# Kernel optimization log

Hardware: AMD Instinct MI355X
Metric: run time of the kernel (lower is better)

The kernel has to match this reference:

```python
import jax, jax.numpy as jnp
import numpy as np

B, N, E = 16, 512, 131072
FEAT, EMB, H = 3, 512, 3
K1, K2 = 410, 205  # ceil(0.8*512), ceil(0.5*410) per PyG TopKPooling
NEG_SLOPE, EPS = 0.2, 1e-5


def _gat_conv(x, W, att_s, att_d, bias, src, tgt, valid, num_nodes):
    # PyG GATConv (concat=True): per-edge attention with segment softmax over targets.
    Hh, C = att_s.shape
    xp = (x @ W).reshape(-1, Hh, C)                      # [Nn,H,C]
    a_s = jnp.einsum('nhc,hc->nh', xp, att_s)
    a_d = jnp.einsum('nhc,hc->nh', xp, att_d)
    srcc = jnp.where(valid, src, 0)
    tgtc = jnp.where(valid, tgt, 0)
    e = jax.nn.leaky_relu(a_s[srcc] + a_d[tgtc], NEG_SLOPE)  # [Ee,H]
    seg = jnp.where(valid, tgt, num_nodes)               # invalid edges -> dummy segment
    emax = jax.ops.segment_max(e, seg, num_segments=num_nodes + 1)
    emax = jnp.where(jnp.isfinite(emax), emax, 0.0)
    ex = jnp.exp(e - emax[seg]) * valid[:, None].astype(e.dtype)
    den = jax.ops.segment_sum(ex, seg, num_segments=num_nodes + 1)
    alpha = ex / jnp.maximum(den[seg], 1e-16)            # [Ee,H]
    out = jax.ops.segment_sum(alpha[:, :, None] * xp[srcc], seg,
                              num_segments=num_nodes + 1)[:num_nodes]
    return out.reshape(num_nodes, Hh * C) + bias


def _bn(x, g, b):
    # BatchNorm1d, training-mode batch statistics (biased var), eps=1e-5
    m = x.mean(0)
    v = x.var(0)
    return (x - m) * jax.lax.rsqrt(v + EPS) * g + b


def _topk_pool(x, p, nb, n_per, k):
    # PyG TopKPooling: score = tanh(x.w/||w||), keep top-k per graph, scale by score
    score = jnp.tanh((x @ p) / jnp.linalg.norm(p))       # [nb*n_per]
    top_s, top_i = jax.lax.top_k(score.reshape(nb, n_per), k)
    perm = (top_i + jnp.arange(nb)[:, None] * n_per).reshape(-1)
    x_new = x[perm] * top_s.reshape(-1, 1)
    mapping = jnp.full((nb * n_per,), -1, jnp.int32).at[perm].set(
        jnp.arange(nb * k, dtype=jnp.int32))
    return x_new, mapping


def _pool_cat(x, nb, k):
    # [global_max_pool, global_mean_pool] over equal-size graphs
    xr = x.reshape(nb, k, -1)
    return jnp.concatenate([xr.max(1), xr.mean(1)], axis=1)


def _forward(x, W1, as1, ad1, bc1, Wh1, bh1, g1, be1, p1,
             W2, as2, ad2, bc2, Wh2, bh2, g2, be2, p2,
             Wl1, bl1, Wl2, bl2, edge_index):
    Nn = B * N
    src0, tgt0 = edge_index[0], edge_index[1]
    sl = jnp.arange(Nn, dtype=jnp.int32)                 # GATConv add_self_loops=True
    src1 = jnp.concatenate([src0, sl]); tgt1 = jnp.concatenate([tgt0, sl])
    valid1 = jnp.ones(src1.shape, bool)
    h = _gat_conv(x, W1, as1, ad1, bc1, src1, tgt1, valid1, Nn)
    h = jax.nn.relu(h @ Wh1 + bh1)
    h = _bn(h, g1, be1)
    h, mapping = _topk_pool(h, p1, B, N, K1)
    x1 = _pool_cat(h, B, K1)                             # [B, 2*EMB]
    # relabel edges to pooled node ids; drop edges with removed endpoints via mask
    s2 = mapping[src0]; t2 = mapping[tgt0]
    v2 = (s2 >= 0) & (t2 >= 0)
    sl2 = jnp.arange(B * K1, dtype=jnp.int32)
    src2 = jnp.concatenate([s2, sl2]); tgt2 = jnp.concatenate([t2, sl2])
    valid2 = jnp.concatenate([v2, jnp.ones(sl2.shape, bool)])
    h = _gat_conv(h, W2, as2, ad2, bc2, src2, tgt2, valid2, B * K1)
    h = jax.nn.relu(h @ Wh2 + bh2)
    h = _bn(h, g2, be2)
    h, _ = _topk_pool(h, p2, B, K1, K2)
    x2 = _pool_cat(h, B, K2)
    xg = x1 + x2
    xg = jax.nn.relu(xg @ Wl1 + bl1)                     # dropout p=0.5 disabled (eval)
    return xg @ Wl2 + bl2                                # [B, 256]


def setup_inputs() -> dict:
    key = jax.random.key(0)
    ks = jax.random.split(key, 16)
    x = jax.random.normal(ks[0], (B * N, FEAT), jnp.float32)
    goff = jnp.repeat(jnp.arange(B, dtype=jnp.int32), E // B) * N
    src = jax.random.randint(ks[1], (E,), 0, N, jnp.int32) + goff
    tgt = jax.random.randint(ks[2], (E,), 0, N, jnp.int32) + goff
    edge_index = jnp.stack([src, tgt])
    s = 0.05
    p = {
        'W1': jax.random.normal(ks[3], (FEAT, H * EMB)) * s,
        'as1': jax.random.normal(ks[4], (H, EMB)) * s,
        'ad1': jax.random.normal(ks[5], (H, EMB)) * s,
        'bc1': jnp.zeros((H * EMB,)),
        'Wh1': jax.random.normal(ks[6], (H * EMB, EMB)) * s,
        'bh1': jnp.zeros((EMB,)),
        'g1': jnp.ones((EMB,)), 'be1': jnp.zeros((EMB,)),
        'p1': jax.random.normal(ks[7], (EMB,)) * s,
        'W2': jax.random.normal(ks[8], (EMB, H * EMB)) * s,
        'as2': jax.random.normal(ks[9], (H, EMB)) * s,
        'ad2': jax.random.normal(ks[10], (H, EMB)) * s,
        'bc2': jnp.zeros((H * EMB,)),
        'Wh2': jax.random.normal(ks[11], (H * EMB, EMB)) * s,
        'bh2': jnp.zeros((EMB,)),
        'g2': jnp.ones((EMB,)), 'be2': jnp.zeros((EMB,)),
        'p2': jax.random.normal(ks[12], (EMB,)) * s,
        'Wl1': jax.random.normal(ks[13], (2 * EMB, 512)) * s,
        'bl1': jnp.zeros((512,)),
        'Wl2': jax.random.normal(ks[14], (512, 256)) * s,
        'bl2': jnp.zeros((256,)),
    }
    return {'x': x, 'edge_index': edge_index, **p}


def reference(x, edge_index, W1, as1, ad1, bc1, Wh1, bh1, g1, be1, p1,
              W2, as2, ad2, bc2, Wh2, bh2, g2, be2, p2, Wl1, bl1, Wl2, bl2):
    return _forward(x, W1, as1, ad1, bc1, Wh1, bh1, g1, be1, p1,
                    W2, as2, ad2, bc2, Wh2, bh2, g2, be2, p2,
                    Wl1, bl1, Wl2, bl2, edge_index)
```

## Files before the change

### kernel.cpp

```cpp
#include <hip/hip_runtime.h>
#include <hip/hip_bf16.h>
#include <math.h>

#define E_EDGES 131072
#define NN1 8192
#define NN2 6560
#define NG 16
#define NP1 512
#define KP1 410
#define KP2 205
#define F1 1536
#define EMB 512
#define MAXDEG 256
#define BNCH 256

typedef __hip_bfloat16 bf16;
typedef __attribute__((ext_vector_type(8))) short short8;
typedef __attribute__((ext_vector_type(4))) float f32x4;
typedef __attribute__((ext_vector_type(4))) unsigned short us4;

__device__ inline float wred64(float v){
  #pragma unroll
  for (int o = 32; o; o >>= 1) v += __shfl_down(v, o);
  return v;
}
__device__ inline float b2f_raw(unsigned short u){
  return __uint_as_float((unsigned)u << 16);
}
union BFU { bf16 b; unsigned short u; };
__device__ inline unsigned short f2u(float v){ BFU x; x.b = __float2bfloat16(v); return x.u; }

__device__ __forceinline__ void gld16(const void* g, void* l){
  __builtin_amdgcn_global_load_lds(
      (const __attribute__((address_space(1))) void*)g,
      (__attribute__((address_space(3))) void*)l, 16, 0, 0);
}

__device__ inline void split_store(float v, bf16* __restrict__ ph, bf16* __restrict__ pl){
  bf16 hi = __float2bfloat16(v);
  *ph = hi;
  *pl = __float2bfloat16(v - __bfloat162float(hi));
}

__device__ inline void bn_tail(float s, float q, int c, float* __restrict__ stats,
    int M, const float* __restrict__ p, float* __restrict__ pnout){
  float mean = s / (float)M;
  float var = fmaxf(q / (float)M - mean*mean, 0.f);
  stats[c] = mean;
  stats[512+c] = 1.f / sqrtf(var + 1e-5f);
  float v = p[c]; v = v*v;
  v = wred64(v);
  __shared__ float red[8];
  int lane = c & 63, wv = c >> 6;
  if (lane == 0) red[wv] = v;
  __syncthreads();
  if (c == 0){ float sm = 0.f; for (int i = 0; i < 8; i++) sm += red[i]; pnout[0] = sqrtf(sm); }
}

__global__ __launch_bounds__(256) void k_pre(
    const float* __restrict__ W1, const float* __restrict__ as1, const float* __restrict__ ad1,
    const float* __restrict__ Wh1, const float* __restrict__ bc1, const float* __restrict__ bh1,
    const float* __restrict__ W2, const float* __restrict__ as2, const float* __restrict__ ad2,
    const float* __restrict__ Wh2, const float* __restrict__ bc2, const float* __restrict__ bh2,
    float* __restrict__ was1, float* __restrict__ wad1, float* __restrict__ M1p,
    float* __restrict__ cvp,
    float* __restrict__ was2, float* __restrict__ wad2,
    int* __restrict__ cnt1, int* __restrict__ cnt2, int* __restrict__ map,
    float* __restrict__ bnacc, float* __restrict__ bnacc1){
  int b = blockIdx.x, t = threadIdx.x;
  if (b < 24){
    int h = b / 8, rem = b % 8, jh = rem >> 2, kc = rem & 3;
    int j = jh*256 + t, c0 = kc*128;
    __shared__ float w1s[3][128];
    for (int i = t; i < 384; i += 256)
      w1s[i>>7][i&127] = W1[(i>>7)*1536 + h*512 + c0 + (i&127)];
    __syncthreads();
    const float* whc = Wh1 + (size_t)(h*512 + c0)*512 + j;
    float a0=0.f, a1=0.f, a2=0.f;
    #pragma unroll 8
    for (int c = 0; c < 128; c++){
      float v = whc[(size_t)c*512];
      a0 += w1s[0][c]*v; a1 += w1s[1][c]*v; a2 += w1s[2][c]*v;
    }
    float* dst = M1p + (size_t)kc*4608;
    dst[(h*3+0)*512 + j] = a0;
    dst[(h*3+1)*512 + j] = a1;
    dst[(h*3+2)*512 + j] = a2;
  } else if (b < 56){
    int b2 = b - 24;
    int which = b2 >> 4, rem = b2 & 15, jh = rem >> 3, kc = rem & 7;
    const float* bc = which ? bc2 : bc1;
    const float* Wh = which ? Wh2 : Wh1;
    const float* bh = which ? bh2 : bh1;
    int j = jh*256 + t, i0 = kc*192;
    float acc = (kc == 0) ? bh[j] : 0.f;
    #pragma unroll 8
    for (int i = 0; i < 192; i++)
      acc += bc[i0+i] * Wh[(size_t)(i0+i)*512 + j];
    cvp[(size_t)(which*8 + kc)*512 + j] = acc;
  } else if (b < 152){
    int b3 = b - 56;
    int y = b3 >> 4, et = b3 & 15;
    int kind = y / 3, h = y % 3;
    int w = t >> 6, lane = t & 63;
    const float* att = kind ? ad2 : as2;
    float a[8];
    #pragma unroll
    for (int u = 0; u < 8; u++) a[u] = att[h*512 + lane*8 + u];
    for (int r = w; r < 32; r += 4){
      int e = et*32 + r;
      const float4* row = (const float4*)(W2 + (size_t)e*1536 + h*512) + lane*2;
      float4 v0 = row[0], v1 = row[1];
      float d = v0.x*a[0]+v0.y*a[1]+v0.z*a[2]+v0.w*a[3]
              + v1.x*a[4]+v1.y*a[5]+v1.z*a[6]+v1.w*a[7];
      d = wred64(d);
      if (lane == 0) (kind ? wad2 : was2)[h*512 + e] = d;
    }
  } else if (b < 170){
    if (t < 64){
      int bb = b - 152;
      int kind = bb / 9, r = bb % 9, h = r / 3, f = r % 3;
      const float* att = kind ? ad1 : as1;
      float s = 0.f;
      for (int c = t; c < 512; c += 64) s += W1[f*1536 + h*512 + c] * att[h*512 + c];
      s = wred64(s);
      if (t == 0) (kind ? wad1 : was1)[h*3 + f] = s;
    }
  } else {
    int i = (b - 170)*256 + t;
    if (i < NN1){ cnt1[i] = 1; map[i] = -1; }
    if (i < NN2){ cnt2[i] = 1; }
    if (i < 1024){ bnacc[i] = 0.f; bnacc1[i] = 0.f; }
  }
}

__global__ __launch_bounds__(256) void k_gemm_s_mfma(const float* __restrict__ A0,
    const float* __restrict__ B0, bf16* __restrict__ Th, bf16* __restrict__ Tl){
  int z = blockIdx.z;
  const float* A = A0 + (size_t)z*512;
  const float* B = B0 + (size_t)z*512*512;
  __shared__ __align__(16) short sAh[4096], sAl[4096], sBh[4096], sBl[4096];
  int t = threadIdx.x, w = t >> 6, lane = t & 63;
  int l16 = lane & 15, q = lane >> 4;
  int bm = blockIdx.y*64, bn = blockIdx.x*64;

  int am  = t >> 2, akw = (t & 3)*16;
  int bnl = t & 63, bkq = (t >> 6)*16;

  f32x4 acc[4];
  #pragma unroll
  for (int nf = 0; nf < 4; nf++) acc[nf] = (f32x4){0.f,0.f,0.f,0.f};

  float va[16], vb[16];
  #define GS_LOAD(K0) do { \
    _Pragma("unroll") for (int u = 0; u < 4; u++){ \
      float4 v4 = *(const float4*)(A + (size_t)(bm+am)*1536 + (K0) + akw + u*4); \
      va[u*4]=v4.x; va[u*4+1]=v4.y; va[u*4+2]=v4.z; va[u*4+3]=v4.w; } \
    _Pragma("unroll") for (int u = 0; u < 16; u++) \
      vb[u] = B[(size_t)((K0) + bkq + u)*512 + bn + bnl]; \
  } while(0)

  GS_LOAD(0);
  for (int it = 0; it < 8; it++){
    #pragma unroll
    for (int hh = 0; hh < 2; hh++){
      short8 ah_, al_, bh_, bl_;
      #pragma unroll
      for (int jj = 0; jj < 8; jj++){
        float v = va[hh*8+jj];
        unsigned short hu = f2u(v);
        ah_[jj] = (short)hu; al_[jj] = (short)f2u(v - b2f_raw(hu));
        v = vb[hh*8+jj];
        hu = f2u(v);
        bh_[jj] = (short)hu; bl_[jj] = (short)f2u(v - b2f_raw(hu));
      }
      int aoff = am*64  + ((((akw>>3) + hh) ^ (am  & 7)) << 3);
      *(short8*)(sAh + aoff) = ah_;
      *(short8*)(sAl + aoff) = al_;
      int boff = bnl*64 + ((((bkq>>3) + hh) ^ (bnl & 7)) << 3);
      *(short8*)(sBh + boff) = bh_;
      *(short8*)(sBl + boff) = bl_;
    }
    __syncthreads();
    if (it < 7) GS_LOAD((it+1)*64);
    #pragma unroll
    for (int ks = 0; ks < 2; ks++){
      int gc = ks*4 + q;
      int ar = w*16 + l16;
      int ao = ar*64 + ((gc ^ (ar & 7)) << 3);
      short8 afh = *(const short8*)(sAh + ao);
      short8 afl = *(const short8*)(sAl + ao);
      #pragma unroll
      for (int nf = 0; nf < 4; nf++){
        int br = nf*16 + l16;
        int bo = br*64 + ((gc ^ (br & 7)) << 3);
        short8 bfh = *(const short8*)(sBh + bo);
        short8 bfl = *(const short8*)(sBl + bo);
        acc[nf] = __builtin_amdgcn_mfma_f32_16x16x32_bf16(afh, bfh, acc[nf], 0, 0, 0);
        acc[nf] = __builtin_amdgcn_mfma_f32_16x16x32_bf16(afh, bfl, acc[nf], 0, 0, 0);
        acc[nf] = __builtin_amdgcn_mfma_f32_16x16x32_bf16(afl, bfh, acc[nf], 0, 0, 0);
      }
    }
    __syncthreads();
  }
  #undef GS_LOAD

  int m0 = bm + w*16 + q*4;
  #pragma unroll
  for (int nf = 0; nf < 4; nf++){
    int n = bn + nf*16 + l16;
    size_t base = (size_t)n*1536 + (size_t)z*512 + m0;
    #pragma unroll
    for (int e = 0; e < 4; e++)
      split_store(acc[nf][e], &Th[base+e], &Tl[base+e]);
  }
}

__global__ void k_count1(const int* __restrict__ tgt0, int* __restrict__ cnt, int E){
  int i = blockIdx.x*blockDim.x + threadIdx.x;
  if (i < E) atomicAdd(&cnt[tgt0[i]], 1);
}
__global__ void k_count2(const int* __restrict__ src0, const int* __restrict__ tgt0,
                         const int* __restrict__ map, int* __restrict__ cnt, int E){
  int i = blockIdx.x*blockDim.x + threadIdx.x;
  if (i >= E) return;
  int s = map[src0[i]], tg = map[tgt0[i]];
  if (s >= 0 && tg >= 0) atomicAdd(&cnt[tg], 1);
}
__global__ __launch_bounds__(1024) void k_scan(const int* __restrict__ counts,
    int* __restrict__ off, int* __restrict__ cur, int n){
  __shared__ int sh[1024];
  int t = threadIdx.x;
  int chunk = (n + 1023) >> 10;
  int b = t * chunk; int e = b + chunk; if (e > n) e = n;
  int s = 0;
  for (int i = b; i < e && i < n; i++) s += counts[i];
  sh[t] = s; __syncthreads();
  for (int o = 1; o < 1024; o <<= 1){
    int v = (t >= o) ? sh[t-o] : 0;
    __syncthreads();
    sh[t] += v;
    __syncthreads();
  }
  int run = (t > 0) ? sh[t-1] : 0;
  for (int i = b; i < e && i < n; i++){ int c = counts[i]; off[i] = run; cur[i] = run; run += c; }
  if (t == 1023) off[n] = sh[1023];
}
__global__ void k_fill1(const int* __restrict__ src0, const int* __restrict__ tgt0,
                        int* __restrict__ cur, int* __restrict__ esrc, int E, int nn){
  int i = blockIdx.x*blockDim.x + threadIdx.x;
  if (i >= E + nn) return;
  int s, tg;
  if (i < E){ s = src0[i]; tg = tgt0[i]; } else { s = i - E; tg = s; }
  int pos = atomicAdd(&cur[tg], 1);
  esrc[pos] = s;
}
__global__ void k_fill2(const int* __restrict__ src0, const int* __restrict__ tgt0,
                        const int* __restrict__ map, int* __restrict__ cur,
                        int* __restrict__ esrc, int E, int nn){
  int i = blockIdx.x*blockDim.x + threadIdx.x;
  if (i >= E + nn) return;
  int s, tg;
  if (i < E){
    s = map[src0[i]]; tg = map[tgt0[i]];
    if (s < 0 || tg < 0) return;
  } else { s = i - E; tg = s; }
  int pos = atomicAdd(&cur[tg], 1);
  esrc[pos] = s;
}

__global__ __launch_bounds__(64) void k_agg1(
    const float* __restrict__ x, const int* __restrict__ off, const int* __restrict__ esrc,
    const float* __restrict__ was, const float* __restrict__ wad,
    float* __restrict__ aggx){
  int n = blockIdx.x, t = threadIdx.x;
  __shared__ float xs[MAXDEG][3];
  __shared__ float al[MAXDEG*3];
  __shared__ float mh[3], dh[3];
  int s0 = off[n]; int deg = off[n+1] - s0; if (deg > MAXDEG) deg = MAXDEG;
  float ad0, ad1, ad2;
  {
    float x0 = x[n*3], x1 = x[n*3+1], x2 = x[n*3+2];
    ad0 = x0*wad[0] + x1*wad[1] + x2*wad[2];
    ad1 = x0*wad[3] + x1*wad[4] + x2*wad[5];
    ad2 = x0*wad[6] + x1*wad[7] + x2*wad[8];
  }
  for (int e = t; e < deg; e += 64){
    int s = esrc[s0 + e];
    float x0 = x[s*3], x1 = x[s*3+1], x2 = x[s*3+2];
    xs[e][0] = x0; xs[e][1] = x1; xs[e][2] = x2;
    float v0 = x0*was[0] + x1*was[1] + x2*was[2] + ad0;
    float v1 = x0*was[3] + x1*was[4] + x2*was[5] + ad1;
    float v2 = x0*was[6] + x1*was[7] + x2*was[8] + ad2;
    al[e*3+0] = v0 > 0.f ? v0 : 0.2f*v0;
    al[e*3+1] = v1 > 0.f ? v1 : 0.2f*v1;
    al[e*3+2] = v2 > 0.f ? v2 : 0.2f*v2;
  }
  __syncthreads();
  if (t < 3){
    float m = -INFINITY;
    for (int e = 0; e < deg; e++) m = fmaxf(m, al[e*3+t]);
    float d = 0.f;
    for (int e = 0; e < deg; e++) d += expf(al[e*3+t] - m);
    mh[t] = m; dh[t] = 1.f / fmaxf(d, 1e-16f);
  }
  __syncthreads();
  float acc[9] = {0,0,0,0,0,0,0,0,0};
  for (int e = t; e < deg; e += 64){
    #pragma unroll
    for (int h = 0; h < 3; h++){
      float a = expf(al[e*3+h] - mh[h]) * dh[h];
      acc[h*3+0] += a * xs[e][0];
      acc[h*3+1] += a * xs[e][1];
      acc[h*3+2] += a * xs[e][2];
    }
  }
  #pragma unroll
  for (int q = 0; q < 9; q++){
    float v = wred64(acc[q]);
    if (t == 0) aggx[(size_t)n*9 + q] = v;
  }
}

__global__ __launch_bounds__(256) void k_h1(const float* __restrict__ aggx,
    const float* __restrict__ M1p, const float* __restrict__ cvp1, bf16* __restrict__ hout,
    float* __restrict__ bnacc1){
  __shared__ float sM[9*512];
  __shared__ float sC[512];
  __shared__ float sA[32*9];
  int t = threadIdx.x; int n0 = blockIdx.x*32;
  for (int i = t; i < 9*512; i += 256)
    sM[i] = M1p[i] + M1p[4608 + i] + M1p[2*4608 + i] + M1p[3*4608 + i];
  for (int i = t; i < 512; i += 256){
    float s = 0.f;
    #pragma unroll
    for (int kc = 0; kc < 8; kc++) s += cvp1[kc*512 + i];
    sC[i] = s;
  }
  for (int i = t; i < 288; i += 256) sA[i] = aggx[(size_t)n0*9 + i];
  __syncthreads();
  float c0v = sC[t], c1v = sC[t+256];
  float ls0=0.f, lq0=0.f, ls1=0.f, lq1=0.f;
  #pragma unroll 4
  for (int i = 0; i < 32; i++){
    float a0 = c0v, a1 = c1v;
    #pragma unroll
    for (int q = 0; q < 9; q++){
      float av = sA[i*9+q];
      a0 += av * sM[q*512 + t];
      a1 += av * sM[q*512 + t + 256];
    }
    a0 = fmaxf(a0, 0.f); a1 = fmaxf(a1, 0.f);
    hout[(size_t)(n0+i)*512 + t]       = __float2bfloat16(a0);
    hout[(size_t)(n0+i)*512 + t + 256] = __float2bfloat16(a1);
    ls0 += a0; lq0 += a0*a0; ls1 += a1; lq1 += a1*a1;
  }
  atomicAdd(&bnacc1[t],           ls0);
  atomicAdd(&bnacc1[t+256],       ls1);
  atomicAdd(&bnacc1[512 + t],     lq0);
  atomicAdd(&bnacc1[512 + t+256], lq1);
}

__global__ void k_bn_final_1(const float* __restrict__ bnacc,
    float* __restrict__ stats, int M, const float* __restrict__ p, float* __restrict__ pnout){
  int c = threadIdx.x;
  bn_tail(bnacc[c], bnacc[512 + c], c, stats, M, p, pnout);
}
__global__ __launch_bounds__(256) void k_score(
    const bf16* __restrict__ h, const float* __restrict__ stats,
    const float* __restrict__ g_, const float* __restrict__ be,
    const float* __restrict__ p, const float* __restrict__ pn,
    float* __restrict__ score){
  int r = blockIdx.x, t = threadIdx.x;
  float dot = 0.f;
  #pragma unroll
  for (int k = 0; k < 2; k++){
    int c = t + k*256;
    float v = (__bfloat162float(h[(size_t)r*EMB + c]) - stats[c]) * stats[512+c] * g_[c] + be[c];
    dot += v * p[c];
  }
  dot = wred64(dot);
  __shared__ float red[4];
  int lane = t & 63, wv = t >> 6;
  if (lane == 0) red[wv] = dot;
  __syncthreads();
  if (t == 0) score[r] = tanhf((red[0]+red[1]+red[2]+red[3]) / pn[0]);
}

__global__ __launch_bounds__(512) void k_topk_sort(
    const float* __restrict__ score, int* __restrict__ map,
    int* __restrict__ topi, float* __restrict__ tops, int n_per, int K){
  int g = blockIdx.x, t = threadIdx.x;
  __shared__ float sk[512];
  __shared__ int si[512];
  if (t < n_per){ sk[t] = score[g*n_per + t]; si[t] = t; }
  else { sk[t] = -INFINITY; si[t] = 0x7fffffff; }
  __syncthreads();
  for (int k = 2; k <= 512; k <<= 1){
    for (int j = k >> 1; j > 0; j >>= 1){
      int l = t ^ j;
      if (l > t){
        float ki = sk[t], kl = sk[l]; int ii = si[t], il = si[l];
        bool before_l = (kl > ki) || (kl == ki && il < ii);
        bool up = ((t & k) == 0);
        if (up == before_l){ sk[t]=kl; sk[l]=ki; si[t]=il; si[l]=ii; }
      }
      __syncthreads();
    }
  }
  if (t < K){
    if (map) map[g*n_per + si[t]] = g*K + t;
    topi[g*K + t] = si[t];
    tops[g*K + t] = sk[t];
  }
}

__global__ __launch_bounds__(256) void k_topk_gather(
    const bf16* __restrict__ h, const float* __restrict__ stats,
    const float* __restrict__ gm, const float* __restrict__ be,
    const int* __restrict__ topi, const float* __restrict__ tops,
    bf16* __restrict__ xn, int n_per, int K,
    const float* __restrict__ was2, const float* __restrict__ wad2,
    float* __restrict__ aso, float* __restrict__ ado){
  int row = blockIdx.x, t = threadIdx.x;
  int gr = row / K, i = row - gr*K;
  int sidx = topi[gr*K + i];
  float s = tops[gr*K + i];
  const bf16* src = h + ((size_t)(gr*n_per + sidx))*EMB;
  bf16* dst = xn + (size_t)row*EMB;
  int c0 = t, c1 = t + 256;
  float v0 = ((__bfloat162float(src[c0]) - stats[c0]) * stats[512+c0] * gm[c0] + be[c0]) * s;
  float v1 = ((__bfloat162float(src[c1]) - stats[c1]) * stats[512+c1] * gm[c1] + be[c1]) * s;
  dst[c0] = __float2bfloat16(v0);
  dst[c1] = __float2bfloat16(v1);
  if (was2){
    float a[6];
    #pragma unroll
    for (int hh = 0; hh < 3; hh++){
      a[hh]   = v0*was2[hh*512 + c0] + v1*was2[hh*512 + c1];
      a[3+hh] = v0*wad2[hh*512 + c0] + v1*wad2[hh*512 + c1];
    }
    __shared__ float red[6][4];
    int lane = t & 63, wv = t >> 6;
    #pragma unroll
    for (int q = 0; q < 6; q++){ float v = wred64(a[q]); if (lane==0) red[q][wv]=v; }
    __syncthreads();
    if (t < 6){
      float sm = red[t][0]+red[t][1]+red[t][2]+red[t][3];
      if (t < 3) aso[row*3+t] = sm; else ado[row*3+(t-3)] = sm;
    }
  }
}

__global__ __launch_bounds__(512) void k_poolA(const bf16* __restrict__ xn,
    float* __restrict__ cat, int K){
  int g = blockIdx.x, c = threadIdx.x;
  const unsigned short* p = (const unsigned short*)xn + (size_t)g*K*EMB + c;
  float mx = -INFINITY, sm = 0.f;
  #pragma unroll 4
  for (int r = 0; r < K; r++){
    float v = b2f_raw(p[(size_t)r*EMB]);
    mx = fmaxf(mx, v); sm += v;
  }
  cat[g*1024 + c] = mx;
  cat[g*1024 + 512 + c] = sm / (float)K;
}
__global__ __launch_bounds__(512) void k_poolB(const bf16* __restrict__ h,
    const float* __restrict__ stats, const float* __restrict__ gm, const float* __restrict__ be,
    const int* __restrict__ topi, const float* __restrict__ tops,
    float* __restrict__ cat, int n_per, int K){
  int g = blockIdx.x, c = threadIdx.x;
  __shared__ int sti[256];
  __shared__ float sts[256];
  for (int r = c; r < K; r += 512){ sti[r] = topi[g*K + r]; sts[r] = tops[g*K + r]; }
  __syncthreads();
  float mean = stats[c], inv = stats[512+c];
  float gg = gm[c], bb = be[c];
  const unsigned short* hp = (const unsigned short*)h;
  float mx = -INFINITY, sm = 0.f;
  #pragma unroll 4
  for (int r = 0; r < K; r++){
    float v = (b2f_raw(hp[(size_t)(g*n_per + sti[r])*EMB + c]) - mean) * inv * gg + bb;
    v *= sts[r];
    mx = fmaxf(mx, v); sm += v;
  }
  cat[g*1024 + c] = mx;
  cat[g*1024 + 512 + c] = sm / (float)K;
}

__global__ __launch_bounds__(256) void k_agg2(
    const bf16* __restrict__ xn, const float* __restrict__ aso, const float* __restrict__ ado,
    const int* __restrict__ off, const int* __restrict__ esrc,
    bf16* __restrict__ oh){
  int n = blockIdx.x, t = threadIdx.x;
  __shared__ int srcs[MAXDEG];
  __shared__ float al[MAXDEG*3];
  __shared__ float mh[3], dh[3];
  int s0 = off[n]; int deg = off[n+1] - s0; if (deg > MAXDEG) deg = MAXDEG;
  for (int e = t; e < deg; e += 256) srcs[e] = esrc[s0 + e];
  __syncthreads();
  float ad0 = ado[n*3+0], ad1 = ado[n*3+1], ad2 = ado[n*3+2];
  for (int e = t; e < deg; e += 256){
    int s = srcs[e];
    float v0 = aso[s*3+0] + ad0, v1 = aso[s*3+1] + ad1, v2 = aso[s*3+2] + ad2;
    al[e*3+0] = v0 > 0.f ? v0 : 0.2f*v0;
    al[e*3+1] = v1 > 0.f ? v1 : 0.2f*v1;
    al[e*3+2] = v2 > 0.f ? v2 : 0.2f*v2;
  }
  __syncthreads();
  if (t < 3){
    float m = -INFINITY;
    for (int e = 0; e < deg; e++) m = fmaxf(m, al[e*3+t]);
    float d = 0.f;
    for (int e = 0; e < deg; e++) d += expf(al[e*3+t] - m);
    mh[t] = m; dh[t] = 1.f / fmaxf(d, 1e-16f);
  }
  __syncthreads();
  for (int e = t; e < deg; e += 256){
    al[e*3+0] = expf(al[e*3+0]-mh[0])*dh[0];
    al[e*3+1] = expf(al[e*3+1]-mh[1])*dh[1];
    al[e*3+2] = expf(al[e*3+2]-mh[2])*dh[2];
  }
  __syncthreads();
  float acc[2][3] = {};
  for (int e = 0; e < deg; e++){
    int s = srcs[e];
    float a0 = al[e*3], a1 = al[e*3+1], a2 = al[e*3+2];
    #pragma unroll
    for (int k = 0; k < 2; k++){
      float v = __bfloat162float(xn[(size_t)s*512 + t + k*256]);
      acc[k][0] += a0*v; acc[k][1] += a1*v; acc[k][2] += a2*v;
    }
  }
  #pragma unroll
  for (int k = 0; k < 2; k++){
    int c = t + k*256;
    #pragma unroll
    for (int h = 0; h < 3; h++)
      oh[(size_t)n*1536 + h*512 + c] = __float2bfloat16(acc[k][h]);
  }
}

__global__ __launch_bounds__(256, 2) void k_gemm_mfma(
    const bf16* __restrict__ Ah,
    const bf16* __restrict__ Bh, const bf16* __restrict__ Bl,
    const float* __restrict__ bias, bf16* __restrict__ C,
    float* __restrict__ bnacc,
    int M, int N, int K, int Mtiles){
  __shared__ __align__(16) unsigned short lds[2][16384];
  int t = threadIdx.x, w = t >> 6, lane = t & 63;
  int q = lane >> 4, l16 = lane & 15;
  int bmi = (int)blockIdx.x % Mtiles, bni = (int)blockIdx.x / Mtiles;
  int bm = bmi * 128, bn = bni * 64;

  int lr = lane >> 3, lc = lane & 7;
  int kg = ((lc ^ lr) & 7) * 8;
  int ro = w*8 + lr;
  int m0 = bm + ro, m1 = bm + 32 + ro, m2 = bm + 64 + ro, m3 = bm + 96 + ro;
  if (m0 >= M) m0 = M-1;  if (m1 >= M) m1 = M-1;
  if (m2 >= M) m2 = M-1;  if (m3 >= M) m3 = M-1;
  int n0 = bn + ro, n1 = bn + 32 + ro;
  const bf16* ptr[8];
  ptr[0] = Ah + (size_t)m0*K + kg;
  ptr[1] = Ah + (size_t)m1*K + kg;
  ptr[2] = Ah + (size_t)m2*K + kg;
  ptr[3] = Ah + (size_t)m3*K + kg;
  ptr[4] = Bh + (size_t)n0*K + kg;
  ptr[5] = Bh + (size_t)n1*K + kg;
  ptr[6] = Bl + (size_t)n0*K + kg;
  ptr[7] = Bl + (size_t)n1*K + kg;
  const int dof[8] = {0, 2048, 4096, 6144, 8192, 10240, 12288, 14336};

  int wm = (w >> 1) * 64, wn = (w & 1) * 32;
  f32x4 acc[4][2];
  #pragma unroll
  for (int i = 0; i < 4; i++)
    #pragma unroll
    for (int j = 0; j < 2; j++)
      acc[i][j] = (f32x4){0.f, 0.f, 0.f, 0.f};

  #pragma unroll
  for (int u = 0; u < 8; u++){
    gld16(ptr[u], &lds[0][dof[u] + w*512]);
    ptr[u] += 64;
  }

  int nit = K >> 6;
  for (int it = 0; it < nit; it++){
    __syncthreads();
    int cur = it & 1;
    if (it + 1 < nit){
      int nxt = cur ^ 1;
      #pragma unroll
      for (int u = 0; u < 8; u++){
        gld16(ptr[u], &lds[nxt][dof[u] + w*512]);
        ptr[u] += 64;
      }
    }
    const unsigned short* L = lds[cur];
    #pragma unroll
    for (int ks = 0; ks < 2; ks++){
      short8 ah[4], bh2[2], bl2[2];
      int gc = ks*4 + q;
      #pragma unroll
      for (int i = 0; i < 4; i++){
        int r = wm + i*16 + l16;
        ah[i] = *(const short8*)(L + r*64 + ((gc ^ (r & 7)) << 3));
      }
      #pragma unroll
      for (int j = 0; j < 2; j++){
        int r = wn + j*16 + l16;
        int so = ((gc ^ (r & 7)) << 3);
        bh2[j] = *(const short8*)(L + 8192  + r*64 + so);
        bl2[j] = *(const short8*)(L + 12288 + r*64 + so);
      }
      #pragma unroll
      for (int i = 0; i < 4; i++)
        #pragma unroll
        for (int j = 0; j < 2; j++){
          acc[i][j] = __builtin_amdgcn_mfma_f32_16x16x32_bf16(ah[i], bh2[j], acc[i][j], 0, 0, 0);
          acc[i][j] = __builtin_amdgcn_mfma_f32_16x16x32_bf16(ah[i], bl2[j], acc[i][j], 0, 0, 0);
        }
    }
  }

  __syncthreads();
  float* cs = (float*)&lds[0][0];
  float* cq = cs + 128;
  int slot = w >> 1;
  #pragma unroll
  for (int j = 0; j < 2; j++){
    int c_local = wn + j*16 + l16;
    int c = bn + c_local;
    float bv = 0.f;
    if (bias){
      #pragma unroll
      for (int kc = 0; kc < 8; kc++) bv += bias[kc*512 + c];
    }
    float ls = 0.f, lq = 0.f;
    #pragma unroll
    for (int i = 0; i < 4; i++){
      int rb = bm + wm + i*16 + q*4;
      #pragma unroll
      for (int e = 0; e < 4; e++){
        int r = rb + e;
        if (r < M){
          float v = fmaxf(acc[i][j][e] + bv, 0.f);
          C[(size_t)r*N + c] = __float2bfloat16(v);
          ls += v; lq += v*v;
        }
      }
    }
    ls += __shfl_xor(ls, 16); ls += __shfl_xor(ls, 32);
    lq += __shfl_xor(lq, 16); lq += __shfl_xor(lq, 32);
    if (q == 0){ cs[slot*64 + c_local] = ls; cq[slot*64 + c_local] = lq; }
  }
  __syncthreads();
  if (t < 64){
    atomicAdd(&bnacc[bn + t],        cs[t] + cs[64 + t]);
    atomicAdd(&bnacc[512 + bn + t],  cq[t] + cq[64 + t]);
  }
}

__global__ __launch_bounds__(256) void k_head1(const float* __restrict__ c1,
    const float* __restrict__ c2, const float* __restrict__ Wl1,
    const float* __restrict__ bl1, float* __restrict__ t1){
  int g = blockIdx.y;
  int jj = threadIdx.x & 63, kc = threadIdx.x >> 6;
  int j = blockIdx.x*64 + jj;
  float acc = 0.f;
  for (int k = kc*256; k < kc*256 + 256; k++){
    float xg = c1[g*1024 + k] + c2[g*1024 + k];
    acc += xg * Wl1[(size_t)k*512 + j];
  }
  __shared__ float red[4][64];
  red[kc][jj] = acc;
  __syncthreads();
  if (kc == 0){
    float v = red[0][jj]+red[1][jj]+red[2][jj]+red[3][jj] + bl1[j];
    t1[g*512 + j] = fmaxf(v, 0.f);
  }
}
__global__ __launch_bounds__(256) void k_head2(const float* __restrict__ t1,
    const float* __restrict__ Wl2, const float* __restrict__ bl2, float* __restrict__ out){
  int g = blockIdx.y;
  int jj = threadIdx.x & 63, kc = threadIdx.x >> 6;
  int j = blockIdx.x*64 + jj;
  float acc = 0.f;
  for (int k = kc*128; k < kc*128 + 128; k++)
    acc += t1[g*512 + k] * Wl2[(size_t)k*256 + j];
  __shared__ float red[4][64];
  red[kc][jj] = acc;
  __syncthreads();
  if (kc == 0)
    out[g*256 + j] = red[0][jj]+red[1][jj]+red[2][jj]+red[3][jj] + bl2[j];
}

extern "C" void kernel_launch(void* const* d_in, const int* in_sizes, int n_in,
                              void* d_out, int out_size, void* d_ws, size_t ws_size,
                              hipStream_t stream){
  const float* x   = (const float*)d_in[0];
  const int*   ei  = (const int*)d_in[1];
  const float* W1  = (const float*)d_in[2];
  const float* as1 = (const float*)d_in[3];
  const float* ad1 = (const float*)d_in[4];
  const float* bc1 = (const float*)d_in[5];
  const float* Wh1 = (const float*)d_in[6];
  const float* bh1 = (const float*)d_in[7];
  const float* g1  = (const float*)d_in[8];
  const float* be1 = (const float*)d_in[9];
  const float* p1  = (const float*)d_in[10];
  const float* W2  = (const float*)d_in[11];
  const float* as2 = (const float*)d_in[12];
  const float* ad2 = (const float*)d_in[13];
  const float* bc2 = (const float*)d_in[14];
  const float* Wh2 = (const float*)d_in[15];
  const float* bh2 = (const float*)d_in[16];
  const float* g2  = (const float*)d_in[17];
  const float* be2 = (const float*)d_in[18];
  const float* p2  = (const float*)d_in[19];
  const float* Wl1 = (const float*)d_in[20];
  const float* bl1 = (const float*)d_in[21];
  const float* Wl2 = (const float*)d_in[22];
  const float* bl2 = (const float*)d_in[23];
  float* out = (float*)d_out;

  const int* src0 = ei;
  const int* tgt0 = ei + E_EDGES;

  bf16* Cc     = (bf16*)d_ws;
  bf16* xn1    = Cc + (size_t)NN1*EMB;
  bf16* xn2    = xn1 + (size_t)NN2*EMB;
  float* aggx1 = (float*)(xn2 + (size_t)NG*KP2*EMB + 8);
  float* M1    = aggx1 + (size_t)NN1*9;
  float* was2  = M1 + 9*EMB;
  float* wad2  = was2 + 3*EMB;
  float* cvec1 = wad2 + 3*EMB;
  float* cvec2 = cvec1 + EMB;
  float* was1  = cvec2 + EMB;
  float* wad1  = was1 + 16;
  float* bnpsum= wad1 + 16;
  float* bnpsq = bnpsum + (size_t)BNCH*EMB;
  float* stats = bnpsq + (size_t)BNCH*EMB;
  float* bnacc = stats + 1024;
  float* pn    = bnacc + 1024;
  float* score = pn + 16;
  float* cat1  = score + NN1;
  float* cat2  = cat1 + NG*1024;
  float* t1h   = cat2 + NG*1024;
  float* pmax  = t1h + NG*EMB;
  float* psum  = pmax + NG*16*EMB;
  float* aso2  = psum + NG*16*EMB;
  float* ado2  = aso2 + NN2*3;
  float* tops  = ado2 + NN2*3;
  bf16* aggx2h = (bf16*)(tops + NG*KP1);
  bf16* M2Th   = aggx2h + (size_t)NN2*F1;
  bf16* M2Tl   = M2Th + (size_t)EMB*F1;
  int* map     = (int*)(M2Tl + (size_t)EMB*F1);
  int* cnt1    = map + NN1;
  int* off1    = cnt1 + NN1;
  int* cur1    = off1 + NN1 + 8;
  int* esrc1   = cur1 + NN1;
  int* cnt2    = esrc1 + (E_EDGES + NN1);
  int* off2    = cnt2 + NN2;
  int* cur2    = off2 + NN2 + 8;
  int* esrc2   = cur2 + NN2;
  int* topi    = esrc2 + 137700;

  float* bnacc1 = bnpsum;
  float* M1p    = bnpsq;
  float* cvp    = bnpsq + 4*4608;
  float* cvp2   = cvp + 8*512;

  k_pre<<<202,256,0,stream>>>(W1,as1,ad1,Wh1,bc1,bh1, W2,as2,ad2,Wh2,bc2,bh2,
                              was1,wad1,M1p,cvp,was2,wad2,
                              cnt1,cnt2,map,bnacc,bnacc1);
  k_gemm_s_mfma<<<dim3(8,8,3),256,0,stream>>>(W2,Wh2,M2Th,M2Tl);

  k_count1<<<(E_EDGES+255)/256,256,0,stream>>>(tgt0,cnt1,E_EDGES);
  k_scan<<<1,1024,0,stream>>>(cnt1,off1,cur1,NN1);
  k_fill1<<<(E_EDGES+NN1+255)/256,256,0,stream>>>(src0,tgt0,cur1,esrc1,E_EDGES,NN1);
  k_agg1<<<NN1,64,0,stream>>>(x,off1,esrc1,was1,wad1,aggx1);
  k_h1<<<NN1/32,256,0,stream>>>(aggx1,M1p,cvp,Cc,bnacc1);
  k_bn_final_1<<<1,512,0,stream>>>(bnacc1,stats,NN1,p1,pn);
  k_score<<<NN1,256,0,stream>>>(Cc,stats,g1,be1,p1,pn,score);
  k_topk_sort<<<NG,512,0,stream>>>(score,map,topi,tops,NP1,KP1);
  k_topk_gather<<<NG*KP1,256,0,stream>>>(Cc,stats,g1,be1,topi,tops,xn1,NP1,KP1,
      was2,wad2,aso2,ado2);
  k_poolA<<<NG,512,0,stream>>>(xn1,cat1,KP1);

  k_count2<<<(E_EDGES+255)/256,256,0,stream>>>(src0,tgt0,map,cnt2,E_EDGES);
  k_scan<<<1,1024,0,stream>>>(cnt2,off2,cur2,NN2);
  k_fill2<<<(E_EDGES+NN2+255)/256,256,0,stream>>>(src0,tgt0,map,cur2,esrc2,E_EDGES,NN2);
  k_agg2<<<NN2,256,0,stream>>>(xn1,aso2,ado2,off2,esrc2,aggx2h);
  k_gemm_mfma<<<52*8,256,0,stream>>>(aggx2h,M2Th,M2Tl,cvp2,Cc,bnacc,NN2,EMB,F1,52);
  k_bn_final_1<<<1,512,0,stream>>>(bnacc,stats,NN2,p2,pn+1);
  k_score<<<NN2,256,0,stream>>>(Cc,stats,g2,be2,p2,pn+1,score);
  k_topk_sort<<<NG,512,0,stream>>>(score,(int*)nullptr,topi,tops,KP1,KP2);
  k_poolB<<<NG,512,0,stream>>>(Cc,stats,g2,be2,topi,tops,cat2,KP1,KP2);

  k_head1<<<dim3(8,NG),256,0,stream>>>(cat1,cat2,Wl1,bl1,t1h);
  k_head2<<<dim3(4,NG),256,0,stream>>>(t1h,Wl2,bl2,out);
}
```

Before: 377.2 us.

## Merge small launches into neighbouring kernels and widen pooling kernels

Folds the edge-count passes into the tail blocks of the weight GEMM and the top-k gather kernels. The second prefix scan becomes an extra block of the first pooling kernel. The separate BN finalize kernels are removed by recomputing mean and inverse std from the accumulators inside each consumer, which also recomputes the projection norm per block. The pooling kernels now split columns across 4 blocks of 1024 threads with a shared-memory reduction, instead of one 512-thread block per graph. This cuts launch count and serial tiny kernels, at the cost of redundant per-block BN and norm math.

Result: faster. 341.1 us (-9.6%).

```diff
diff --git a/kernel.cpp b/kernel.cpp
--- a/kernel.cpp
+++ b/kernel.cpp
@@ -42,19 +42,11 @@
   *pl = __float2bfloat16(v - __bfloat162float(hi));
 }
 
-__device__ inline void bn_tail(float s, float q, int c, float* __restrict__ stats,
-    int M, const float* __restrict__ p, float* __restrict__ pnout){
-  float mean = s / (float)M;
-  float var = fmaxf(q / (float)M - mean*mean, 0.f);
-  stats[c] = mean;
-  stats[512+c] = 1.f / sqrtf(var + 1e-5f);
-  float v = p[c]; v = v*v;
-  v = wred64(v);
-  __shared__ float red[8];
-  int lane = c & 63, wv = c >> 6;
-  if (lane == 0) red[wv] = v;
-  __syncthreads();
-  if (c == 0){ float sm = 0.f; for (int i = 0; i < 8; i++) sm += red[i]; pnout[0] = sqrtf(sm); }
+__device__ inline void bn_from_acc(const float* __restrict__ bnacc, int c, float fM,
+                                   float& mean, float& inv){
+  mean = bnacc[c] / fM;
+  float var = fmaxf(bnacc[512+c]/fM - mean*mean, 0.f);
+  inv = 1.f / sqrtf(var + 1e-5f);
 }
 
 __global__ __launch_bounds__(256) void k_pre(
@@ -134,15 +126,22 @@
   }
 }
 
-__global__ __launch_bounds__(256) void k_gemm_s_mfma(const float* __restrict__ A0,
-    const float* __restrict__ B0, bf16* __restrict__ Th, bf16* __restrict__ Tl){
-  int z = blockIdx.z;
+__global__ __launch_bounds__(256) void k_gemm_s_c1(const float* __restrict__ A0,
+    const float* __restrict__ B0, bf16* __restrict__ Th, bf16* __restrict__ Tl,
+    const int* __restrict__ tgt0, int* __restrict__ cnt1){
+  int b = blockIdx.x;
+  if (b >= 192){
+    int i = (b - 192)*256 + threadIdx.x;
+    if (i < E_EDGES) atomicAdd(&cnt1[tgt0[i]], 1);
+    return;
+  }
+  int z = b % 3; int rr = b / 3; int by = rr >> 3, bx = rr & 7;
   const float* A = A0 + (size_t)z*512;
   const float* B = B0 + (size_t)z*512*512;
   __shared__ __align__(16) short sAh[4096], sAl[4096], sBh[4096], sBl[4096];
   int t = threadIdx.x, w = t >> 6, lane = t & 63;
   int l16 = lane & 15, q = lane >> 4;
-  int bm = blockIdx.y*64, bn = blockIdx.x*64;
+  int bm = by*64, bn = bx*64;
 
   int am  = t >> 2, akw = (t & 3)*16;
   int bnl = t & 63, bkq = (t >> 6)*16;
@@ -216,25 +215,13 @@
   }
 }
 
-__global__ void k_count1(const int* __restrict__ tgt0, int* __restrict__ cnt, int E){
-  int i = blockIdx.x*blockDim.x + threadIdx.x;
-  if (i < E) atomicAdd(&cnt[tgt0[i]], 1);
-}
-__global__ void k_count2(const int* __restrict__ src0, const int* __restrict__ tgt0,
-                         const int* __restrict__ map, int* __restrict__ cnt, int E){
-  int i = blockIdx.x*blockDim.x + threadIdx.x;
-  if (i >= E) return;
-  int s = map[src0[i]], tg = map[tgt0[i]];
-  if (s >= 0 && tg >= 0) atomicAdd(&cnt[tg], 1);
-}
-__global__ __launch_bounds__(1024) void k_scan(const int* __restrict__ counts,
-    int* __restrict__ off, int* __restrict__ cur, int n){
-  __shared__ int sh[1024];
+__device__ inline void scan_body(const int* __restrict__ counts, int* __restrict__ off,
+                                 int* __restrict__ cur, int n, int* __restrict__ sh){
   int t = threadIdx.x;
   int chunk = (n + 1023) >> 10;
   int b = t * chunk; int e = b + chunk; if (e > n) e = n;
   int s = 0;
-  for (int i = b; i < e && i < n; i++) s += counts[i];
+  for (int i = b; i < e; i++) s += counts[i];
   sh[t] = s; __syncthreads();
   for (int o = 1; o < 1024; o <<= 1){
     int v = (t >= o) ? sh[t-o] : 0;
@@ -243,8 +230,13 @@
     __syncthreads();
   }
   int run = (t > 0) ? sh[t-1] : 0;
-  for (int i = b; i < e && i < n; i++){ int c = counts[i]; off[i] = run; cur[i] = run; run += c; }
+  for (int i = b; i < e; i++){ int c = counts[i]; off[i] = run; cur[i] = run; run += c; }
   if (t == 1023) off[n] = sh[1023];
+}
+__global__ __launch_bounds__(1024) void k_scan(const int* __restrict__ counts,
+    int* __restrict__ off, int* __restrict__ cur, int n){
+  __shared__ int sh[1024];
+  scan_body(counts, off, cur, n, sh);
 }
 __global__ void k_fill1(const int* __restrict__ src0, const int* __restrict__ tgt0,
                         int* __restrict__ cur, int* __restrict__ esrc, int E, int nn){
@@ -361,30 +353,32 @@
   atomicAdd(&bnacc1[512 + t+256], lq1);
 }
 
-__global__ void k_bn_final_1(const float* __restrict__ bnacc,
-    float* __restrict__ stats, int M, const float* __restrict__ p, float* __restrict__ pnout){
-  int c = threadIdx.x;
-  bn_tail(bnacc[c], bnacc[512 + c], c, stats, M, p, pnout);
-}
 __global__ __launch_bounds__(256) void k_score(
-    const bf16* __restrict__ h, const float* __restrict__ stats,
+    const bf16* __restrict__ h, const float* __restrict__ bnacc, int M,
     const float* __restrict__ g_, const float* __restrict__ be,
-    const float* __restrict__ p, const float* __restrict__ pn,
-    float* __restrict__ score){
+    const float* __restrict__ p, float* __restrict__ score){
   int r = blockIdx.x, t = threadIdx.x;
-  float dot = 0.f;
+  float fM = (float)M;
+  float dot = 0.f, pp = 0.f;
   #pragma unroll
   for (int k = 0; k < 2; k++){
     int c = t + k*256;
-    float v = (__bfloat162float(h[(size_t)r*EMB + c]) - stats[c]) * stats[512+c] * g_[c] + be[c];
-    dot += v * p[c];
-  }
-  dot = wred64(dot);
-  __shared__ float red[4];
+    float mean, inv; bn_from_acc(bnacc, c, fM, mean, inv);
+    float v = (__bfloat162float(h[(size_t)r*EMB + c]) - mean) * inv * g_[c] + be[c];
+    float pc = p[c];
+    dot += v * pc;
+    pp += pc * pc;
+  }
+  dot = wred64(dot); pp = wred64(pp);
+  __shared__ float red[4], redp[4];
   int lane = t & 63, wv = t >> 6;
-  if (lane == 0) red[wv] = dot;
-  __syncthreads();
-  if (t == 0) score[r] = tanhf((red[0]+red[1]+red[2]+red[3]) / pn[0]);
+  if (lane == 0){ red[wv] = dot; redp[wv] = pp; }
+  __syncthreads();
+  if (t == 0){
+    float d = red[0]+red[1]+red[2]+red[3];
+    float pn = sqrtf(redp[0]+redp[1]+redp[2]+redp[3]);
+    score[r] = tanhf(d / pn);
+  }
 }
 
 __global__ __launch_bounds__(512) void k_topk_sort(
@@ -415,25 +409,39 @@
   }
 }
 
-__global__ __launch_bounds__(256) void k_topk_gather(
-    const bf16* __restrict__ h, const float* __restrict__ stats,
+__global__ __launch_bounds__(256) void k_gather_c2(
+    const bf16* __restrict__ h, const float* __restrict__ bnacc, int M,
     const float* __restrict__ gm, const float* __restrict__ be,
     const int* __restrict__ topi, const float* __restrict__ tops,
     bf16* __restrict__ xn, int n_per, int K,
     const float* __restrict__ was2, const float* __restrict__ wad2,
-    float* __restrict__ aso, float* __restrict__ ado){
+    float* __restrict__ aso, float* __restrict__ ado,
+    const int* __restrict__ src0, const int* __restrict__ tgt0,
+    const int* __restrict__ map, int* __restrict__ cnt2, int nblk_g){
   int row = blockIdx.x, t = threadIdx.x;
+  if (row >= nblk_g){
+    int i = (row - nblk_g)*256 + t;
+    if (i < E_EDGES){
+      int s = map[src0[i]], tg = map[tgt0[i]];
+      if (s >= 0 && tg >= 0) atomicAdd(&cnt2[tg], 1);
+    }
+    return;
+  }
   int gr = row / K, i = row - gr*K;
   int sidx = topi[gr*K + i];
   float s = tops[gr*K + i];
   const bf16* src = h + ((size_t)(gr*n_per + sidx))*EMB;
   bf16* dst = xn + (size_t)row*EMB;
   int c0 = t, c1 = t + 256;
-  float v0 = ((__bfloat162float(src[c0]) - stats[c0]) * stats[512+c0] * gm[c0] + be[c0]) * s;
-  float v1 = ((__bfloat162float(src[c1]) - stats[c1]) * stats[512+c1] * gm[c1] + be[c1]) * s;
+  float fM = (float)M;
+  float mean0, inv0, mean1, inv1;
+  bn_from_acc(bnacc, c0, fM, mean0, inv0);
+  bn_from_acc(bnacc, c1, fM, mean1, inv1);
+  float v0 = ((__bfloat162float(src[c0]) - mean0) * inv0 * gm[c0] + be[c0]) * s;
+  float v1 = ((__bfloat162float(src[c1]) - mean1) * inv1 * gm[c1] + be[c1]) * s;
   dst[c0] = __float2bfloat16(v0);
   dst[c1] = __float2bfloat16(v1);
-  if (was2){
+  {
     float a[6];
     #pragma unroll
     for (int hh = 0; hh < 3; hh++){
@@ -452,40 +460,65 @@
   }
 }
 
-__global__ __launch_bounds__(512) void k_poolA(const bf16* __restrict__ xn,
-    float* __restrict__ cat, int K){
-  int g = blockIdx.x, c = threadIdx.x;
-  const unsigned short* p = (const unsigned short*)xn + (size_t)g*K*EMB + c;
+__global__ __launch_bounds__(1024) void k_poolA_scan(const bf16* __restrict__ xn,
+    float* __restrict__ cat, int K,
+    const int* __restrict__ cnt2, int* __restrict__ off2, int* __restrict__ cur2){
+  __shared__ int shi[1024];
+  __shared__ float smax[8][128];
+  __shared__ float ssum[8][128];
+  int b = blockIdx.x, t = threadIdx.x;
+  if (b == 64){ scan_body(cnt2, off2, cur2, NN2, shi); return; }
+  int g = b >> 2, cb = b & 3;
+  int c = t & 127, rg = t >> 7;
+  int col = cb*128 + c;
+  const unsigned short* p = (const unsigned short*)xn + (size_t)g*K*EMB + col;
   float mx = -INFINITY, sm = 0.f;
-  #pragma unroll 4
-  for (int r = 0; r < K; r++){
+  for (int r = rg; r < K; r += 8){
     float v = b2f_raw(p[(size_t)r*EMB]);
     mx = fmaxf(mx, v); sm += v;
   }
-  cat[g*1024 + c] = mx;
-  cat[g*1024 + 512 + c] = sm / (float)K;
-}
-__global__ __launch_bounds__(512) void k_poolB(const bf16* __restrict__ h,
-    const float* __restrict__ stats, const float* __restrict__ gm, const float* __restrict__ be,
+  smax[rg][c] = mx; ssum[rg][c] = sm;
+  __syncthreads();
+  if (rg == 0){
+    #pragma unroll
+    for (int u = 1; u < 8; u++){ mx = fmaxf(mx, smax[u][c]); sm += ssum[u][c]; }
+    cat[g*1024 + col] = mx;
+    cat[g*1024 + 512 + col] = sm / (float)K;
+  }
+}
+__global__ __launch_bounds__(1024) void k_poolB(const bf16* __restrict__ h,
+    const float* __restrict__ bnacc, int M,
+    const float* __restrict__ gm, const float* __restrict__ be,
     const int* __restrict__ topi, const float* __restrict__ tops,
     float* __restrict__ cat, int n_per, int K){
-  int g = blockIdx.x, c = threadIdx.x;
   __shared__ int sti[256];
   __shared__ float sts[256];
-  for (int r = c; r < K; r += 512){ sti[r] = topi[g*K + r]; sts[r] = tops[g*K + r]; }
-  __syncthreads();
-  float mean = stats[c], inv = stats[512+c];
-  float gg = gm[c], bb = be[c];
+  __shared__ float smax[8][128];
+  __shared__ float ssum[8][128];
+  int b = blockIdx.x, t = threadIdx.x;
+  int g = b >> 2, cb = b & 3;
+  for (int r = t; r < K; r += 1024){ sti[r] = topi[g*K + r]; sts[r] = tops[g*K + r]; }
+  __syncthreads();
+  int c = t & 127, rg = t >> 7;
+  int col = cb*128 + c;
+  float fM = (float)M;
+  float mean, inv; bn_from_acc(bnacc, col, fM, mean, inv);
+  float gg = gm[col], bb = be[col];
   const unsigned short* hp = (const unsigned short*)h;
   float mx = -INFINITY, sm = 0.f;
-  #pragma unroll 4
-  for (int r = 0; r < K; r++){
-    float v = (b2f_raw(hp[(size_t)(g*n_per + sti[r])*EMB + c]) - mean) * inv * gg + bb;
+  for (int r = rg; r < K; r += 8){
+    float v = (b2f_raw(hp[(size_t)(g*n_per + sti[r])*EMB + col]) - mean) * inv * gg + bb;
     v *= sts[r];
     mx = fmaxf(mx, v); sm += v;
   }
-  cat[g*1024 + c] = mx;
-  cat[g*1024 + 512 + c] = sm / (float)K;
+  smax[rg][c] = mx; ssum[rg][c] = sm;
+  __syncthreads();
+  if (rg == 0){
+    #pragma unroll
+    for (int u = 1; u < 8; u++){ mx = fmaxf(mx, smax[u][c]); sm += ssum[u][c]; }
+    cat[g*1024 + col] = mx;
+    cat[g*1024 + 512 + col] = sm / (float)K;
+  }
 }
 
 __global__ __launch_bounds__(256) void k_agg2(
@@ -775,29 +808,24 @@
   k_pre<<<202,256,0,stream>>>(W1,as1,ad1,Wh1,bc1,bh1, W2,as2,ad2,Wh2,bc2,bh2,
                               was1,wad1,M1p,cvp,was2,wad2,
                               cnt1,cnt2,map,bnacc,bnacc1);
-  k_gemm_s_mfma<<<dim3(8,8,3),256,0,stream>>>(W2,Wh2,M2Th,M2Tl);
-
-  k_count1<<<(E_EDGES+255)/256,256,0,stream>>>(tgt0,cnt1,E_EDGES);
+  k_gemm_s_c1<<<704,256,0,stream>>>(W2,Wh2,M2Th,M2Tl,tgt0,cnt1);
+
   k_scan<<<1,1024,0,stream>>>(cnt1,off1,cur1,NN1);
   k_fill1<<<(E_EDGES+NN1+255)/256,256,0,stream>>>(src0,tgt0,cur1,esrc1,E_EDGES,NN1);
   k_agg1<<<NN1,64,0,stream>>>(x,off1,esrc1,was1,wad1,aggx1);
   k_h1<<<NN1/32,256,0,stream>>>(aggx1,M1p,cvp,Cc,bnacc1);
-  k_bn_final_1<<<1,512,0,stream>>>(bnacc1,stats,NN1,p1,pn);
-  k_score<<<NN1,256,0,stream>>>(Cc,stats,g1,be1,p1,pn,score);
+  k_score<<<NN1,256,0,stream>>>(Cc,bnacc1,NN1,g1,be1,p1,score);
   k_topk_sort<<<NG,512,0,stream>>>(score,map,topi,tops,NP1,KP1);
-  k_topk_gather<<<NG*KP1,256,0,stream>>>(Cc,stats,g1,be1,topi,tops,xn1,NP1,KP1,
-      was2,wad2,aso2,ado2);
-  k_poolA<<<NG,512,0,stream>>>(xn1,cat1,KP1);
-
-  k_count2<<<(E_EDGES+255)/256,256,0,stream>>>(src0,tgt0,map,cnt2,E_EDGES);
-  k_scan<<<1,1024,0,stream>>>(cnt2,off2,cur2,NN2);
+  k_gather_c2<<<NG*KP1+512,256,0,stream>>>(Cc,bnacc1,NN1,g1,be1,topi,tops,xn1,NP1,KP1,
+      was2,wad2,aso2,ado2, src0,tgt0,map,cnt2,NG*KP1);
+  k_poolA_scan<<<65,1024,0,stream>>>(xn1,cat1,KP1, cnt2,off2,cur2);
+
   k_fill2<<<(E_EDGES+NN2+255)/256,256,0,stream>>>(src0,tgt0,map,cur2,esrc2,E_EDGES,NN2);
   k_agg2<<<NN2,256,0,stream>>>(xn1,aso2,ado2,off2,esrc2,aggx2h);
   k_gemm_mfma<<<52*8,256,0,stream>>>(aggx2h,M2Th,M2Tl,cvp2,Cc,bnacc,NN2,EMB,F1,52);
-  k_bn_final_1<<<1,512,0,stream>>>(bnacc,stats,NN2,p2,pn+1);
-  k_score<<<NN2,256,0,stream>>>(Cc,stats,g2,be2,p2,pn+1,score);
+  k_score<<<NN2,256,0,stream>>>(Cc,bnacc,NN2,g2,be2,p2,score);
   k_topk_sort<<<NG,512,0,stream>>>(score,(int*)nullptr,topi,tops,KP1,KP2);
-  k_poolB<<<NG,512,0,stream>>>(Cc,stats,g2,be2,topi,tops,cat2,KP1,KP2);
+  k_poolB<<<64,1024,0,stream>>>(Cc,bnacc,NN2,g2,be2,topi,tops,cat2,KP1,KP2);
 
   k_head1<<<dim3(8,NG),256,0,stream>>>(cat1,cat2,Wl1,bl1,t1h);
   k_head2<<<dim3(4,NG),256,0,stream>>>(t1h,Wl2,bl2,out);
```
